# Kernel optimization log

Hardware: AMD Instinct MI355X
Metric: run time of the kernel (lower is better)

## Reference

```python
import jax, jax.numpy as jnp
import numpy as np

B, S, D = 2, 2048, 768
H = 12
DEPTH = D // H
DFF = 4 * D
EPS = 1e-5


def setup_inputs() -> dict:
    key = jax.random.key(0)
    ks = jax.random.split(key, 9)
    sd = 0.02
    return {
        "x": jax.random.normal(ks[0], (B, S, D), dtype=jnp.float32),
        "Wqkv": jax.random.normal(ks[1], (D, 3 * D), dtype=jnp.float32) * sd,
        "Wout": jax.random.normal(ks[2], (D, D), dtype=jnp.float32) * sd,
        "bout": jnp.zeros((D,), dtype=jnp.float32),
        "W1": jax.random.normal(ks[3], (D, DFF), dtype=jnp.float32) * sd,
        "b1": jnp.zeros((DFF,), dtype=jnp.float32),
        "W2": jax.random.normal(ks[4], (DFF, D), dtype=jnp.float32) * sd,
        "b2": jnp.zeros((D,), dtype=jnp.float32),
        "g1": jnp.ones((D,), dtype=jnp.float32),
        "be1": jnp.zeros((D,), dtype=jnp.float32),
        "g2": jnp.ones((D,), dtype=jnp.float32),
        "be2": jnp.zeros((D,), dtype=jnp.float32),
    }


def _layernorm(x, gain, bias):
    mean = jnp.mean(x, axis=-1, keepdims=True)
    var = jnp.mean(jnp.square(x - mean), axis=-1, keepdims=True)  # unbiased=False
    return gain * (x - mean) / jnp.sqrt(var + EPS) + bias


def reference(x, Wqkv, Wout, bout, W1, b1, W2, b2, g1, be1, g2, be2):
    b, s, d = x.shape
    # QKV projection (no bias), chunk into q,k,v
    qkv = jnp.einsum("bsd,de->bse", x, Wqkv)
    q, k, v = jnp.split(qkv, 3, axis=-1)
    q = q.reshape(b, s, H, DEPTH).transpose(0, 2, 1, 3)  # bhsd
    k = k.reshape(b, s, H, DEPTH).transpose(0, 2, 1, 3)
    v = v.reshape(b, s, H, DEPTH).transpose(0, 2, 1, 3)
    scores = jnp.einsum("bhqd,bhkd->bhqk", q, k) / np.sqrt(DEPTH).astype(np.float32)
    # causal mask (use_masking=True)
    causal = jnp.tril(jnp.ones((s, s), dtype=bool))
    scores = jnp.where(causal, scores, -jnp.inf)
    attn = jax.nn.softmax(scores, axis=-1)
    ctx = jnp.einsum("bhqk,bhkd->bhqd", attn, v)
    ctx = ctx.transpose(0, 2, 1, 3).reshape(b, s, d)
    attn_out = jnp.einsum("bsd,de->bse", ctx, Wout) + bout
    # residual + LN1 (dropout is identity in eval)
    h = _layernorm(x + attn_out, g1, be1)
    # FFN
    ff = jax.nn.relu(jnp.einsum("bsd,df->bsf", h, W1) + b1)
    ff = jnp.einsum("bsf,fd->bsd", ff, W2) + b2
    return _layernorm(h + ff, g2, be2)
```

## Files before the change

### kernel.cpp

```cpp
#include <hip/hip_runtime.h>


typedef __attribute__((ext_vector_type(8)))  short    short8;
typedef __attribute__((ext_vector_type(4)))  float    floatx4;
typedef __attribute__((ext_vector_type(16))) float    floatx16;
typedef __attribute__((ext_vector_type(4)))  unsigned uint4v;

#define QSC 0.18033688f
#define C2  24.0f

__device__ __forceinline__ float b2f(unsigned short u) {
    return __uint_as_float(((unsigned)u) << 16);
}
__device__ __forceinline__ unsigned short f2b(float f) {
    unsigned x = __float_as_uint(f);
    return (unsigned short)((x + 0x7fffu + ((x >> 16) & 1u)) >> 16);
}
__device__ __forceinline__ void async_cp16(const void* g, void* l) {
    __builtin_amdgcn_global_load_lds((const __attribute__((address_space(1))) void*)g,
                                     (__attribute__((address_space(3))) void*)l,
                                     16, 0, 0);
}
__device__ __forceinline__ unsigned cvtpk(float lo, float hi) {
    unsigned r;
    asm("v_cvt_pk_bf16_f32 %0, %1, %2" : "=v"(r) : "v"(lo), "v"(hi));
    return r;
}
__device__ __forceinline__ void plswap(unsigned& a, unsigned& b) {
    asm("v_permlane32_swap_b32 %0, %1" : "+v"(a), "+v"(b));
}
__device__ __forceinline__ int chunk_ofs8(int qb) {
    int t = qb >> 2, rem = qb & 3;
    return (t + 1) * (2 * t + rem);
}
__device__ __forceinline__ int swz16(int row, int chunk) {
    return row * 64 + (((chunk ^ (row & 7)) & 7) << 3);
}

__global__ __launch_bounds__(256) void prep_all(
    const float* __restrict__ x,    unsigned short* __restrict__ xb,
    const float* __restrict__ Wqkv, unsigned short* __restrict__ wqkvT,
    const float* __restrict__ Wout, unsigned short* __restrict__ woutT,
    const float* __restrict__ W1,   unsigned short* __restrict__ w1T,
    const float* __restrict__ W2,   unsigned short* __restrict__ w2T)
{
    __shared__ float tile[32][33];
    int idx = blockIdx.x;
    int tx = threadIdx.x & 31, ty = threadIdx.x >> 5;
    if (idx >= 6912) {
        int i = (idx - 6912) * 256 + threadIdx.x;
        float4 v = ((const float4*)x)[i];
        ushort4 u;
        u.x = f2b(v.x); u.y = f2b(v.y); u.z = f2b(v.z); u.w = f2b(v.w);
        ((ushort4*)xb)[i] = u;
        return;
    }
    const float* W; unsigned short* Wt; int K, N, bx, by;
    if (idx < 1728)      { W = Wqkv; Wt = wqkvT; K = 768;  N = 2304; bx = idx % 72;        by = idx / 72; }
    else if (idx < 2304) { W = Wout; Wt = woutT; K = 768;  N = 768;  bx = (idx-1728) % 24; by = (idx-1728) / 24; }
    else if (idx < 4608) { W = W1;   Wt = w1T;   K = 768;  N = 3072; bx = (idx-2304) % 96; by = (idx-2304) / 96; }
    else                 { W = W2;   Wt = w2T;   K = 3072; N = 768;  bx = (idx-4608) % 24; by = (idx-4608) / 24; }
    int n0 = bx * 32, k0 = by * 32;
    for (int i = ty; i < 32; i += 8)
        tile[i][tx] = W[(size_t)(k0 + i) * N + n0 + tx];
    __syncthreads();
    for (int i = ty; i < 32; i += 8)
        Wt[(size_t)(n0 + i) * K + k0 + tx] = f2b(tile[tx][i]);
}

__global__ __launch_bounds__(256) void gemm_bf16(
    const unsigned short* __restrict__ A,
    const unsigned short* __restrict__ Bt,
    const float* __restrict__ bias,
    float* __restrict__ outF,
    unsigned short* __restrict__ outB,
    int M, int N, int K, int relu, int mode, int kslab)
{
    __shared__ unsigned short As[8192];
    __shared__ unsigned short Bs[8192];
    const int tid  = threadIdx.x;
    const int m0   = blockIdx.y * 128;
    const int n0   = blockIdx.x * 128;
    const int kz   = blockIdx.z;
    const int kbeg = kz * kslab;
    const int kend = kbeg + kslab;
    const int lane = tid & 63;
    const int wave = tid >> 6;
    const int wm   = (wave >> 1) * 64;
    const int wn   = (wave & 1) * 64;
    const int fr   = lane & 15;
    const int fq   = lane >> 4;

    floatx4 acc[4][4];
    for (int i = 0; i < 4; i++)
        for (int j = 0; j < 4; j++)
            for (int e = 0; e < 4; e++) acc[i][j][e] = 0.f;

    for (int kk = kbeg; kk < kend; kk += 64) {
        __syncthreads();
        #pragma unroll
        for (int r = 0; r < 4; ++r) {
            int c   = r * 256 + tid;
            int row = c >> 3;
            int jj  = ((c & 7) ^ (row & 7)) * 8;
            async_cp16(A  + (size_t)(m0 + row) * K + kk + jj, &As[c * 8]);
            async_cp16(Bt + (size_t)(n0 + row) * K + kk + jj, &Bs[c * 8]);
        }
        __syncthreads();

        #pragma unroll
        for (int kc = 0; kc < 2; ++kc) {
            short8 a[4], b[4];
            #pragma unroll
            for (int t = 0; t < 4; t++) a[t] = *(const short8*)&As[swz16(wm + t * 16 + fr, kc * 4 + fq)];
            #pragma unroll
            for (int t = 0; t < 4; t++) b[t] = *(const short8*)&Bs[swz16(wn + t * 16 + fr, kc * 4 + fq)];
            #pragma unroll
            for (int i = 0; i < 4; i++)
                #pragma unroll
                for (int j = 0; j < 4; j++)
                    acc[i][j] = __builtin_amdgcn_mfma_f32_16x16x32_bf16(a[i], b[j], acc[i][j], 0, 0, 0);
        }
    }

    if (mode == 2) {
        float* dst = outF + (size_t)kz * M * N;
        #pragma unroll
        for (int j = 0; j < 4; j++) {
            int col = n0 + wn + j * 16 + fr;
            #pragma unroll
            for (int i = 0; i < 4; i++) {
                int rbase = m0 + wm + i * 16 + fq * 4;
                #pragma unroll
                for (int e = 0; e < 4; e++)
                    dst[(size_t)(rbase + e) * N + col] = acc[i][j][e];
            }
        }
        return;
    }
    if (mode == 1) {
        #pragma unroll
        for (int j = 0; j < 4; j++) {
            int col   = n0 + wn + j * 16 + fr;
            int which = (col >= 1536) ? 2 : (col >= 768 ? 1 : 0);
            float sc  = (which == 0) ? QSC : 1.0f;
            int rem   = col - which * 768;
            int hh    = rem >> 6, d = rem & 63;
            #pragma unroll
            for (int i = 0; i < 4; i++) {
                int rbase = m0 + wm + i * 16 + fq * 4;
                #pragma unroll
                for (int e = 0; e < 4; e++) {
                    int row = rbase + e;
                    int b_  = row >> 11, srow = row & 2047;
                    size_t idx = (size_t)which * 3145728 +
                                 ((size_t)(b_ * 12 + hh) * 2048 + srow) * 64 + d;
                    outB[idx] = f2b(acc[i][j][e] * sc);
                }
            }
        }
        return;
    }
    #pragma unroll
    for (int j = 0; j < 4; j++) {
        int col  = n0 + wn + j * 16 + fr;
        float bv = bias ? bias[col] : 0.f;
        #pragma unroll
        for (int i = 0; i < 4; i++) {
            int rbase = m0 + wm + i * 16 + fq * 4;
            #pragma unroll
            for (int e = 0; e < 4; e++) {
                float v = acc[i][j][e] + bv;
                if (relu) v = fmaxf(v, 0.f);
                size_t idx = (size_t)(rbase + e) * N + col;
                if (outF) outF[idx] = v;
                if (outB) outB[idx] = f2b(v);
            }
        }
    }
}

__global__ __launch_bounds__(256, 4) void attn_part(const unsigned short* __restrict__ Qg,
                                                    const unsigned short* __restrict__ Kg,
                                                    const unsigned short* __restrict__ Vg,
                                                    unsigned short* __restrict__ pO,
                                                    float* __restrict__ pL) {
    __shared__ unsigned short Ks[2][4096];
    __shared__ unsigned short Vt[2][4096];
    const int tid  = threadIdx.x;
    const int lane = tid & 63;
    const int wave = tid >> 6;
    const int ql   = lane & 31;
    const int hi   = lane >> 5;
    const int wm   = wave * 32;
    const int r    = 39 - blockIdx.x;
    const int bh   = blockIdx.y;
    int qb = 0;
    for (int q_ = 15; q_ >= 0; --q_) if (r >= chunk_ofs8(q_)) { qb = q_; break; }
    const int c     = r - chunk_ofs8(qb);
    const int q0    = qb * 128;
    const int tile0 = 8 * c;
    const int ntk   = min(8, 2 * (qb + 1) - 8 * c);
    const int slot  = bh * 40 + r;
    const unsigned short* Qb = Qg + (size_t)bh * 131072;
    const unsigned short* Kb = Kg + (size_t)bh * 131072;
    const unsigned short* Vb = Vg + (size_t)bh * 131072;
    const int qrow = q0 + wm + ql;

    short8 qf[4];
    {
        const unsigned short* qr = Qb + (size_t)qrow * 64 + hi * 8;
        #pragma unroll
        for (int c4 = 0; c4 < 4; ++c4)
            qf[c4] = *(const short8*)(qr + c4 * 16);
    }

    floatx16 o[2];
    #pragma unroll
    for (int db = 0; db < 2; ++db)
        #pragma unroll
        for (int e = 0; e < 16; ++e) o[db][e] = 0.f;
    float ls[4] = {0.f, 0.f, 0.f, 0.f};

    const int c0 = tid, c1 = tid + 256;
    uint4 kr0, kr1, vr0, vr1;

#define LOADT(TG)                                                              \
    {                                                                          \
        int base = (TG) * 64;                                                  \
        kr0 = *(const uint4*)(Kb + (size_t)(base + (c0 >> 3)) * 64 + (c0 & 7) * 8); \
        kr1 = *(const uint4*)(Kb + (size_t)(base + (c1 >> 3)) * 64 + (c1 & 7) * 8); \
        vr0 = *(const uint4*)(Vb + (size_t)(base + (c0 & 63)) * 64 + (c0 >> 6) * 8); \
        vr1 = *(const uint4*)(Vb + (size_t)(base + (c1 & 63)) * 64 + (c1 >> 6) * 8); \
    }
#define WRITET(BUF)                                                            \
    {                                                                          \
        *(uint4*)&Ks[BUF][swz16(c0 >> 3, c0 & 7)] = kr0;                       \
        *(uint4*)&Ks[BUF][swz16(c1 >> 3, c1 & 7)] = kr1;                       \
        unsigned short t0[8]; *(uint4*)t0 = vr0;                               \
        _Pragma("unroll") for (int i_ = 0; i_ < 8; ++i_)                       \
            Vt[BUF][((c0 >> 6) * 8 + i_) * 64 +                                \
                    (((((c0 >> 3) & 7) ^ i_) << 3) | (c0 & 7))] = t0[i_];      \
        unsigned short t1[8]; *(uint4*)t1 = vr1;                               \
        _Pragma("unroll") for (int i_ = 0; i_ < 8; ++i_)                       \
            Vt[BUF][((c1 >> 6) * 8 + i_) * 64 +                                \
                    (((((c1 >> 3) & 7) ^ i_) << 3) | (c1 & 7))] = t1[i_];      \
    }

    LOADT(tile0);
    WRITET(0);
    __syncthreads();

    for (int kt = 0; kt < ntk; ++kt) {
        const int  tg   = tile0 + kt;
        const int  cur  = kt & 1;
        const bool more = (kt + 1 < ntk);
        if (more) LOADT(tg + 1);

        #pragma unroll
        for (int bb = 0; bb < 2; ++bb) {
            short8 kf[4];
            #pragma unroll
            for (int c4 = 0; c4 < 4; ++c4)
                kf[c4] = *(const short8*)&Ks[cur][swz16(32 * bb + ql, 2 * c4 + hi)];
            floatx16 s;
            #pragma unroll
            for (int e = 0; e < 16; ++e) s[e] = 0.f;
            #pragma unroll
            for (int c4 = 0; c4 < 4; ++c4)
                s = __builtin_amdgcn_mfma_f32_32x32x16_bf16(kf[c4], qf[c4], s, 0, 0, 0);

            const int  kvb = tg * 64 + 32 * bb + 4 * hi;
            const bool nm  = (tg * 64 + 32 * bb + 31) > (q0 + wm);
            if (nm) {
                #pragma unroll
                for (int e = 0; e < 16; ++e)
                    if (kvb + (e & 3) + 8 * (e >> 2) > qrow) s[e] = -1e30f;
            }
            float pv[16];
            #pragma unroll
            for (int e = 0; e < 16; ++e) {
                pv[e] = __builtin_amdgcn_exp2f(s[e] - C2);
                ls[e & 3] += pv[e];
            }

            unsigned w[8];
            #pragma unroll
            for (int m = 0; m < 4; ++m) {
                w[2 * m]     = cvtpk(pv[4 * m],     pv[4 * m + 1]);
                w[2 * m + 1] = cvtpk(pv[4 * m + 2], pv[4 * m + 3]);
            }
            plswap(w[0], w[2]);
            plswap(w[1], w[3]);
            plswap(w[4], w[6]);
            plswap(w[5], w[7]);
            uint4v u0 = {w[0], w[1], w[2], w[3]};
            uint4v u1 = {w[4], w[5], w[6], w[7]};
            short8 pa0 = __builtin_bit_cast(short8, u0);
            short8 pa1 = __builtin_bit_cast(short8, u1);

            #pragma unroll
            for (int db = 0; db < 2; ++db) {
                short8 vf0 = *(const short8*)&Vt[cur][swz16(32 * db + ql, 4 * bb + hi)];
                short8 vf1 = *(const short8*)&Vt[cur][swz16(32 * db + ql, 4 * bb + 2 + hi)];
                o[db] = __builtin_amdgcn_mfma_f32_32x32x16_bf16(pa0, vf0, o[db], 0, 0, 0);
                o[db] = __builtin_amdgcn_mfma_f32_32x32x16_bf16(pa1, vf1, o[db], 0, 0, 0);
            }
        }

        if (more) {
            WRITET(cur ^ 1);
            __syncthreads();
        }
    }
#undef LOADT
#undef WRITET

    float lsum = (ls[0] + ls[1]) + (ls[2] + ls[3]);
    lsum += __shfl_xor(lsum, 32);
    #pragma unroll
    for (int db = 0; db < 2; ++db)
        #pragma unroll
        for (int e = 0; e < 16; ++e) {
            int row = wm + (e & 3) + 8 * (e >> 2) + 4 * hi;
            pO[((size_t)slot * 128 + row) * 64 + db * 32 + ql] = f2b(o[db][e]);
        }
    if (lane < 32)
        pL[(size_t)slot * 128 + wm + ql] = lsum;
}

__global__ __launch_bounds__(256) void attn_combine(const unsigned short* __restrict__ pO,
                                                    const float* __restrict__ pL,
                                                    unsigned short* __restrict__ ctx) {
    const int qb  = blockIdx.x;
    const int bh  = blockIdx.y;
    const int b   = bh / 12, h = bh % 12;
    const int nch = (qb >> 2) + 1;
    const int slot0 = bh * 40 + chunk_ofs8(qb);
    const int tid = threadIdx.x;
    const int row = tid >> 1;
    const int col0 = (tid & 1) * 32;

    float L = 0.f;
    for (int i = 0; i < nch; ++i)
        L += pL[(size_t)(slot0 + i) * 128 + row];

    float acc[32];
    #pragma unroll
    for (int j = 0; j < 32; ++j) acc[j] = 0.f;
    for (int i = 0; i < nch; ++i) {
        const unsigned short* p = pO + ((size_t)(slot0 + i) * 128 + row) * 64 + col0;
        #pragma unroll
        for (int v4 = 0; v4 < 4; ++v4) {
            uint4 u = *(const uint4*)(p + v4 * 8);
            unsigned short t[8]; *(uint4*)t = u;
            #pragma unroll
            for (int j = 0; j < 8; ++j) acc[v4 * 8 + j] += b2f(t[j]);
        }
    }
    float inv = 1.f / L;
    unsigned short* orow = ctx + ((size_t)(b * 2048 + qb * 128 + row)) * 768 + h * 64 + col0;
    #pragma unroll
    for (int v4 = 0; v4 < 4; ++v4) {
        unsigned short t[8];
        #pragma unroll
        for (int j = 0; j < 8; ++j) t[j] = f2b(acc[v4 * 8 + j] * inv);
        *(uint4*)(orow + v4 * 8) = *(uint4*)t;
    }
}

__global__ __launch_bounds__(256) void resid_ln2(const float* __restrict__ X,
                                                 const float* __restrict__ P,
                                                 int nsplit,
                                                 const float* __restrict__ bv,
                                                 const float* __restrict__ gain,
                                                 const float* __restrict__ beta,
                                                 float* __restrict__ outF,
                                                 unsigned short* __restrict__ outB) {
    const int row = blockIdx.x;
    const int t   = threadIdx.x;
    const size_t off = (size_t)row * 768;
    float v[3];
    #pragma unroll
    for (int i = 0; i < 3; i++) {
        size_t c = off + t + i * 256;
        float r = X[c] + bv[t + i * 256];
        for (int p = 0; p < nsplit; ++p) r += P[(size_t)p * 3145728 + c];
        v[i] = r;
    }
    float s  = v[0] + v[1] + v[2];
    float s2 = v[0] * v[0] + v[1] * v[1] + v[2] * v[2];
    #pragma unroll
    for (int o2 = 32; o2 > 0; o2 >>= 1) {
        s  += __shfl_down(s,  o2);
        s2 += __shfl_down(s2, o2);
    }
    __shared__ float rs[4], rq[4];
    if ((t & 63) == 0) { rs[t >> 6] = s; rq[t >> 6] = s2; }
    __syncthreads();
    float S    = rs[0] + rs[1] + rs[2] + rs[3];
    float S2   = rq[0] + rq[1] + rq[2] + rq[3];
    float mean = S * (1.0f / 768.0f);
    float var  = S2 * (1.0f / 768.0f) - mean * mean;
    float inv  = rsqrtf(var + 1e-5f);
    #pragma unroll
    for (int i = 0; i < 3; i++) {
        int c   = t + i * 256;
        float y = gain[c] * (v[i] - mean) * inv + beta[c];
        if (outF) outF[off + c] = y;
        if (outB) outB[off + c] = f2b(y);
    }
}

extern "C" void kernel_launch(void* const* d_in, const int* in_sizes, int n_in,
                              void* d_out, int out_size, void* d_ws, size_t ws_size,
                              hipStream_t stream) {
    const float* x    = (const float*)d_in[0];
    const float* Wqkv = (const float*)d_in[1];
    const float* Wout = (const float*)d_in[2];
    const float* bout = (const float*)d_in[3];
    const float* W1   = (const float*)d_in[4];
    const float* b1   = (const float*)d_in[5];
    const float* W2   = (const float*)d_in[6];
    const float* b2   = (const float*)d_in[7];
    const float* g1   = (const float*)d_in[8];
    const float* be1  = (const float*)d_in[9];
    const float* g2   = (const float*)d_in[10];
    const float* be2  = (const float*)d_in[11];
    float* out = (float*)d_out;

    char* ws = (char*)d_ws;
    unsigned short* wqkvT  = (unsigned short*)(ws + 0);
    unsigned short* woutT  = (unsigned short*)(ws + 3538944);
    unsigned short* w1T    = (unsigned short*)(ws + 4718592);
    unsigned short* w2T    = (unsigned short*)(ws + 9437184);
    unsigned short* xb     = (unsigned short*)(ws + 14155776);
    unsigned short* qkvG   = (unsigned short*)(ws + 20447232);
    unsigned short* Qg     = qkvG;
    unsigned short* Kg     = qkvG + 3145728;
    unsigned short* Vg     = qkvG + 6291456;
    unsigned short* pO     = (unsigned short*)(ws + 39321600);
    float*          pL     = (float*)(ws + 67633152);
    unsigned short* ctxb   = (unsigned short*)(ws + 14155776);
    float*          WoutP  = (float*)(ws + 39321600);
    float*          h      = (float*)(ws + 20447232);
    unsigned short* hb     = (unsigned short*)(ws + 77070336);
    unsigned short* ffb    = (unsigned short*)(ws + 39321600);
    float*          W2P    = (float*)(ws + 64487424);

    prep_all<<<9984, 256, 0, stream>>>(x, xb, Wqkv, wqkvT, Wout, woutT, W1, w1T, W2, w2T);
    gemm_bf16<<<dim3(18, 32), 256, 0, stream>>>(xb, wqkvT, nullptr, nullptr, qkvG,
                                                4096, 2304, 768, 0, 1, 768);
    attn_part<<<dim3(40, 24), 256, 0, stream>>>(Qg, Kg, Vg, pO, pL);
    attn_combine<<<dim3(16, 24), 256, 0, stream>>>(pO, pL, ctxb);
    gemm_bf16<<<dim3(6, 32, 3), 256, 0, stream>>>(ctxb, woutT, nullptr, WoutP, nullptr,
                                                  4096, 768, 768, 0, 2, 256);
    resid_ln2<<<4096, 256, 0, stream>>>(x, WoutP, 3, bout, g1, be1, h, hb);
    gemm_bf16<<<dim3(24, 32), 256, 0, stream>>>(hb, w1T, b1, nullptr, ffb,
                                                4096, 3072, 768, 1, 0, 768);
    gemm_bf16<<<dim3(6, 32, 2), 256, 0, stream>>>(ffb, w2T, nullptr, W2P, nullptr,
                                                  4096, 768, 3072, 0, 2, 1536);
    resid_ln2<<<4096, 256, 0, stream>>>(h, W2P, 2, b2, g2, be2, out, nullptr);
}
```

Measured before the change: 314.1 us.

## Refine LDS swizzle, remap attention block order, stage output through LDS

Three changes to the attention partial kernel. The K/V LDS swizzle gains an extra XOR term to reduce bank conflicts on MFMA operand reads. The block index is remapped so neighbouring blocks spread across heads and chunks, which may balance load across XCDs and caches. The per-element 2-byte global stores of the partial output are replaced by staging in LDS and writing coalesced 16-byte rows, at the cost of two extra barriers.

```diff
diff --git a/kernel.cpp b/kernel.cpp
--- a/kernel.cpp
+++ b/kernel.cpp
@@ -35,6 +35,9 @@
 }
 __device__ __forceinline__ int swz16(int row, int chunk) {
     return row * 64 + (((chunk ^ (row & 7)) & 7) << 3);
+}
+__device__ __forceinline__ int swzB(int row, int chunk) {
+    return row * 64 + (((chunk ^ (row & 7) ^ ((row >> 2) & 6)) & 7) << 3);
 }
 
 __global__ __launch_bounds__(256) void prep_all(
@@ -193,8 +196,10 @@
     const int ql   = lane & 31;
     const int hi   = lane >> 5;
     const int wm   = wave * 32;
-    const int r    = 39 - blockIdx.x;
-    const int bh   = blockIdx.y;
+    const int bid  = blockIdx.y * 40 + blockIdx.x;
+    const int swz  = (bid & 7) * 120 + (bid >> 3);
+    const int bh   = swz / 40;
+    const int r    = 39 - (swz % 40);
     int qb = 0;
     for (int q_ = 15; q_ >= 0; --q_) if (r >= chunk_ofs8(q_)) { qb = q_; break; }
     const int c     = r - chunk_ofs8(qb);
@@ -235,16 +240,18 @@
     }
 #define WRITET(BUF)                                                            \
     {                                                                          \
-        *(uint4*)&Ks[BUF][swz16(c0 >> 3, c0 & 7)] = kr0;                       \
-        *(uint4*)&Ks[BUF][swz16(c1 >> 3, c1 & 7)] = kr1;                       \
+        *(uint4*)&Ks[BUF][swzB(c0 >> 3, c0 & 7)] = kr0;                       \
+        *(uint4*)&Ks[BUF][swzB(c1 >> 3, c1 & 7)] = kr1;                       \
         unsigned short t0[8]; *(uint4*)t0 = vr0;                               \
-        _Pragma("unroll") for (int i_ = 0; i_ < 8; ++i_)                       \
-            Vt[BUF][((c0 >> 6) * 8 + i_) * 64 +                                \
-                    (((((c0 >> 3) & 7) ^ i_) << 3) | (c0 & 7))] = t0[i_];      \
+        _Pragma("unroll") for (int i_ = 0; i_ < 8; ++i_) {                     \
+            int rv = (c0 >> 6) * 8 + i_;                                       \
+            Vt[BUF][rv * 64 + (((((c0 >> 3) & 7) ^ i_ ^ ((rv >> 2) & 6)) & 7) << 3) + (c0 & 7)] = t0[i_]; \
+        }                                                                      \
         unsigned short t1[8]; *(uint4*)t1 = vr1;                               \
-        _Pragma("unroll") for (int i_ = 0; i_ < 8; ++i_)                       \
-            Vt[BUF][((c1 >> 6) * 8 + i_) * 64 +                                \
-                    (((((c1 >> 3) & 7) ^ i_) << 3) | (c1 & 7))] = t1[i_];      \
+        _Pragma("unroll") for (int i_ = 0; i_ < 8; ++i_) {                     \
+            int rv = (c1 >> 6) * 8 + i_;                                       \
+            Vt[BUF][rv * 64 + (((((c1 >> 3) & 7) ^ i_ ^ ((rv >> 2) & 6)) & 7) << 3) + (c1 & 7)] = t1[i_]; \
+        }                                                                      \
     }
 
     LOADT(tile0);
@@ -262,7 +269,7 @@
             short8 kf[4];
             #pragma unroll
             for (int c4 = 0; c4 < 4; ++c4)
-                kf[c4] = *(const short8*)&Ks[cur][swz16(32 * bb + ql, 2 * c4 + hi)];
+                kf[c4] = *(const short8*)&Ks[cur][swzB(32 * bb + ql, 2 * c4 + hi)];
             floatx16 s;
             #pragma unroll
             for (int e = 0; e < 16; ++e) s[e] = 0.f;
@@ -301,8 +308,8 @@
 
             #pragma unroll
             for (int db = 0; db < 2; ++db) {
-                short8 vf0 = *(const short8*)&Vt[cur][swz16(32 * db + ql, 4 * bb + hi)];
-                short8 vf1 = *(const short8*)&Vt[cur][swz16(32 * db + ql, 4 * bb + 2 + hi)];
+                short8 vf0 = *(const short8*)&Vt[cur][swzB(32 * db + ql, 4 * bb + hi)];
+                short8 vf1 = *(const short8*)&Vt[cur][swzB(32 * db + ql, 4 * bb + 2 + hi)];
                 o[db] = __builtin_amdgcn_mfma_f32_32x32x16_bf16(pa0, vf0, o[db], 0, 0, 0);
                 o[db] = __builtin_amdgcn_mfma_f32_32x32x16_bf16(pa1, vf1, o[db], 0, 0, 0);
             }
@@ -318,13 +325,26 @@
 
     float lsum = (ls[0] + ls[1]) + (ls[2] + ls[3]);
     lsum += __shfl_xor(lsum, 32);
+
+    __syncthreads();
+    unsigned short* Ost = &Ks[0][0];
     #pragma unroll
     for (int db = 0; db < 2; ++db)
         #pragma unroll
         for (int e = 0; e < 16; ++e) {
             int row = wm + (e & 3) + 8 * (e >> 2) + 4 * hi;
-            pO[((size_t)slot * 128 + row) * 64 + db * 32 + ql] = f2b(o[db][e]);
-        }
+            int col = db * 32 + ql;
+            Ost[row * 64 + ((((col >> 3) ^ (row & 7)) & 7) << 3) + (col & 7)] =
+                f2b(o[db][e]);
+        }
+    __syncthreads();
+    #pragma unroll
+    for (int p = 0; p < 4; ++p) {
+        int chunk = p * 256 + tid;
+        int row = chunk >> 3, cc = chunk & 7;
+        uint4 val = *(const uint4*)&Ost[row * 64 + (((cc ^ (row & 7)) & 7) << 3)];
+        *(uint4*)(pO + ((size_t)slot * 128 + row) * 64 + cc * 8) = val;
+    }
     if (lane < 32)
         pL[(size_t)slot * 128 + wm + ql] = lsum;
 }
```

Result: no change. 311.4 us (-0.9%).
